# Optimization experiments

Hardware: AMD Instinct MI355X
Metric: run time of the kernel (lower is better)

The kernel has to match this reference:

```python
import jax, jax.numpy as jnp
import numpy as np

N_HEAD = 16
ROPE_BASE = 10000.0


def _rope_cache(T, head_dim):
    # half-split RoPE: cos/sin of shape [T, head_dim//2]
    half = head_dim // 2
    inv_freq = ROPE_BASE ** (-jnp.arange(half, dtype=jnp.float32) / half)
    angles = jnp.arange(T, dtype=jnp.float32)[:, None] * inv_freq[None, :]  # [T, half]
    return jnp.cos(angles), jnp.sin(angles)


def _apply_rope(x, cos, sin):
    # x: [B, H, T, D]; cos/sin: [T, D//2]
    half = x.shape[-1] // 2
    x1, x2 = x[..., :half], x[..., half:]
    c = cos[None, None, :, :]
    s = sin[None, None, :, :]
    return jnp.concatenate([x1 * c - x2 * s, x1 * s + x2 * c], axis=-1)


def setup_inputs() -> dict:
    key = jax.random.key(0)
    k1, k2, k3 = jax.random.split(key, 3)
    B, T, C = 2, 2048, 1024
    x = jax.random.normal(k1, (B, T, C), dtype=jnp.float32)
    w_attn = jax.random.normal(k2, (C, 3 * C), dtype=jnp.float32) * (C ** -0.5)
    b_attn = jnp.zeros((3 * C,), dtype=jnp.float32)
    w_proj = jax.random.normal(k3, (C, C), dtype=jnp.float32) * (C ** -0.5)
    b_proj = jnp.zeros((C,), dtype=jnp.float32)
    return {"x": x, "w_attn": w_attn, "b_attn": b_attn, "w_proj": w_proj, "b_proj": b_proj}


def reference(x, w_attn, b_attn, w_proj, b_proj):
    B, T, C = x.shape
    H = N_HEAD
    hd = C // H

    qkv = x @ w_attn + b_attn                      # [B, T, 3C] fused QKV
    q, k, v = jnp.split(qkv, 3, axis=-1)
    q = q.reshape(B, T, H, hd).transpose(0, 2, 1, 3)  # [B, H, T, hd]
    k = k.reshape(B, T, H, hd).transpose(0, 2, 1, 3)
    v = v.reshape(B, T, H, hd).transpose(0, 2, 1, 3)

    cos, sin = _rope_cache(T, hd)
    q = _apply_rope(q, cos, sin)
    k = _apply_rope(k, cos, sin)

    scale = 1.0 / jnp.sqrt(jnp.float32(hd))
    att = jnp.einsum("bhqd,bhkd->bhqk", q, k) * scale  # [B, H, T, T]
    causal = jnp.tril(jnp.ones((T, T), dtype=bool))
    att = jnp.where(causal[None, None], att, -jnp.inf)
    att = jax.nn.softmax(att, axis=-1)
    y = jnp.einsum("bhqk,bhkd->bhqd", att, v)          # [B, H, T, hd]
    y = y.transpose(0, 2, 1, 3).reshape(B, T, C)
    return y @ w_proj + b_proj
```

## Files before the change

kernel.cpp:

```cpp
#include <hip/hip_runtime.h>
#include <hip/hip_bf16.h>
#include <cmath>

typedef _Float16 half_t;
typedef half_t half4 __attribute__((ext_vector_type(4)));
typedef half_t half8 __attribute__((ext_vector_type(8)));
typedef float f32x4 __attribute__((ext_vector_type(4)));

#define N_HEADS 16
#define HD      64
#define T_SEQ   2048
#define B_SZ    2
#define C_DIM   1024
#define M_ROWS  (B_SZ * T_SEQ)
#define N_QKV   (3 * C_DIM)
#define QSCALE  0.18033688f

__device__ inline void load_lds16(const half_t* g, half_t* l) {
  __builtin_amdgcn_global_load_lds(
      (const __attribute__((address_space(1))) void*)g,
      (__attribute__((address_space(3))) void*)l, 16, 0, 0);
}

__global__ __launch_bounds__(256) void k_prep(const float* __restrict__ x,
                                              half_t* __restrict__ xb,
                                              const float* __restrict__ wa,
                                              half_t* __restrict__ wT,
                                              const float* __restrict__ wp,
                                              half_t* __restrict__ wpT) {
  __shared__ float tile[64][65];
  int bid = blockIdx.x, tid = threadIdx.x;
  if (bid < 4096) {
    int i = (bid * 256 + tid) * 4;
    float4 v = *(const float4*)(x + i);
    half_t o[4] = {(half_t)v.x, (half_t)v.y, (half_t)v.z, (half_t)v.w};
    *(ulong1*)(xb + i) = *(ulong1*)o;
    return;
  }
  const float* in; half_t* out; int K, N, id;
  if (bid < 4096 + 768) { id = bid - 4096; in = wa; out = wT;  K = 1024; N = 3072; }
  else                  { id = bid - 4864; in = wp; out = wpT; K = 1024; N = 1024; }
  int n0 = (id % (N / 64)) * 64, k0 = (id / (N / 64)) * 64;
  int tx = tid & 63, ty = tid >> 6;
  #pragma unroll
  for (int i = 0; i < 64; i += 4)
    tile[ty + i][tx] = in[(size_t)(k0 + ty + i) * N + n0 + tx];
  __syncthreads();
  #pragma unroll
  for (int i = 0; i < 64; i += 4) {
    int r = ty + i;
    out[(size_t)(n0 + r) * K + k0 + tx] = (half_t)tile[tx][r];
  }
}

template <typename OT, int TN>
__global__ __launch_bounds__(256) void k_gemm(const half_t* __restrict__ A,
                                              const half_t* __restrict__ Bt,
                                              const float* __restrict__ bias,
                                              OT* __restrict__ C,
                                              int M, int N, int K) {
  constexpr int NI = TN / 32;
  __shared__ half_t As[128 * 64];
  __shared__ half_t Bs[TN * 64];
  int tid = threadIdx.x;
  int wave = tid >> 6, lane = tid & 63;
  int lane15 = lane & 15, quad = lane >> 4;
  int wm = (wave >> 1) * 64, wn = (wave & 1) * (TN / 2);
  int bm0 = blockIdx.y * 128, bn0 = blockIdx.x * TN;
  f32x4 acc[4][NI] = {};

  for (int kb = 0; kb < K; kb += 64) {
    const half_t* Ag = A + (size_t)bm0 * K + kb;
    const half_t* Bg = Bt + (size_t)bn0 * K + kb;
    __syncthreads();
    #pragma unroll
    for (int p = 0; p < 4; p++) {
      int fc = wave * 4 * 64 + p * 64 + lane;
      int r = fc >> 3, c = (fc & 7) ^ (r & 7);
      load_lds16(Ag + (size_t)r * K + c * 8, As + (wave * 4 + p) * 512);
    }
    #pragma unroll
    for (int p = 0; p < NI; p++) {
      int fc = wave * NI * 64 + p * 64 + lane;
      int r = fc >> 3, c = (fc & 7) ^ (r & 7);
      load_lds16(Bg + (size_t)r * K + c * 8, Bs + (wave * NI + p) * 512);
    }
    __syncthreads();
    #pragma unroll
    for (int ks = 0; ks < 2; ks++) {
      half8 af[4], bf[NI];
      #pragma unroll
      for (int i = 0; i < 4; i++) {
        int Ra = wm + i * 16 + lane15;
        af[i] = *(const half8*)(As + Ra * 64 + ((ks * 4 + quad) ^ (Ra & 7)) * 8);
      }
      #pragma unroll
      for (int i = 0; i < NI; i++) {
        int Rb = wn + i * 16 + lane15;
        bf[i] = *(const half8*)(Bs + Rb * 64 + ((ks * 4 + quad) ^ (Rb & 7)) * 8);
      }
      #pragma unroll
      for (int mi = 0; mi < 4; mi++)
        #pragma unroll
        for (int ni = 0; ni < NI; ni++)
          acc[mi][ni] = __builtin_amdgcn_mfma_f32_16x16x32_f16(af[mi], bf[ni], acc[mi][ni], 0, 0, 0);
    }
  }
  #pragma unroll
  for (int mi = 0; mi < 4; mi++)
    #pragma unroll
    for (int ni = 0; ni < NI; ni++) {
      int n = bn0 + wn + ni * 16 + lane15;
      float bv = bias[n];
      int mrow = bm0 + wm + mi * 16 + quad * 4;
      #pragma unroll
      for (int r = 0; r < 4; r++)
        C[(size_t)(mrow + r) * N + n] = (OT)(acc[mi][ni][r] + bv);
    }
}

__global__ __launch_bounds__(256) void k_rope(const half_t* __restrict__ qkv,
                                              half_t* __restrict__ Q,
                                              half_t* __restrict__ Ko,
                                              half_t* __restrict__ Vt) {
  __shared__ float vt[64][65];
  int bh = blockIdx.y;
  int b = bh >> 4, h = bh & 15;
  int t0 = blockIdx.x * 64;
  int tid = threadIdx.x;
  int trow = tid >> 5, i = tid & 31;
  float inv = exp2f(-(float)i * (13.287712379549449f / 32.0f));
  #pragma unroll
  for (int p = 0; p < 8; p++) {
    int tloc = p * 8 + trow;
    int t = t0 + tloc;
    const half_t* row = qkv + (size_t)(b * T_SEQ + t) * N_QKV;
    float q1 = (float)row[h * 64 + i],        q2 = (float)row[h * 64 + i + 32];
    float k1 = (float)row[1024 + h * 64 + i], k2 = (float)row[1024 + h * 64 + i + 32];
    float v1 = (float)row[2048 + h * 64 + i], v2 = (float)row[2048 + h * 64 + i + 32];
    float s, c;
    sincosf((float)t * inv, &s, &c);
    size_t base = ((size_t)bh * T_SEQ + t) * HD;
    Q[base + i]       = (half_t)((q1 * c - q2 * s) * QSCALE);
    Q[base + i + 32]  = (half_t)((q1 * s + q2 * c) * QSCALE);
    Ko[base + i]      = (half_t)(k1 * c - k2 * s);
    Ko[base + i + 32] = (half_t)(k1 * s + k2 * c);
    vt[i][tloc]      = v1;
    vt[i + 32][tloc] = v2;
  }
  __syncthreads();
  int d = tid >> 6, tc = tid & 63;
  #pragma unroll
  for (int p = 0; p < 16; p++) {
    int dd = p * 4 + d;
    Vt[((size_t)bh * HD + dd) * T_SEQ + t0 + tc] = (half_t)vt[dd][tc];
  }
}

template <bool DIAG>
__device__ __forceinline__ void tile_mfma(const half_t* __restrict__ Kt,
                                          const half_t* __restrict__ Vt,
                                          half8 bq0, half8 bq1,
                                          f32x4 (&ot)[4], float& l,
                                          int lane15, int quad, int qloc) {
  f32x4 sacc[4];
  #pragma unroll
  for (int s = 0; s < 4; s++) {
    int R_ = s * 16 + lane15;
    half8 ak0 = *(const half8*)(Kt + R_ * 64 + ((quad) ^ (R_ & 7)) * 8);
    half8 ak1 = *(const half8*)(Kt + R_ * 64 + ((4 + quad) ^ (R_ & 7)) * 8);
    f32x4 z = {};
    z = __builtin_amdgcn_mfma_f32_16x16x32_f16(ak0, bq0, z, 0, 0, 0);
    sacc[s] = __builtin_amdgcn_mfma_f32_16x16x32_f16(ak1, bq1, z, 0, 0, 0);
  }
  #pragma unroll
  for (int s = 0; s < 4; s++) {
    half4 bp;
    #pragma unroll
    for (int r = 0; r < 4; r++) {
      float sv = sacc[s][r];
      if (DIAG && (s * 16 + quad * 4 + r > qloc)) sv = -1.0e30f;
      float p = exp2f(fminf(sv, 14.0f));
      l += p;
      bp[r] = (half_t)p;
    }
    #pragma unroll
    for (int nm = 0; nm < 4; nm++) {
      int Rv = nm * 16 + lane15;
      half4 av = *(const half4*)(Vt + Rv * 64 +
                                 ((2 * s + (quad >> 1)) ^ (Rv & 7)) * 8 +
                                 (quad & 1) * 4);
      ot[nm] = __builtin_amdgcn_mfma_f32_16x16x16f16(av, bp, ot[nm], 0, 0, 0);
    }
  }
}

#define STAGE(bb, t_)                                                          \
  {                                                                            \
    int gS = wave >> 3;                                                        \
    int idx = (wave & 7) * 64 + lane;                                          \
    int rr_ = idx >> 3, cc = (idx & 7) ^ (rr_ & 7);                            \
    int j = 2 * (t_) + gS;                                                     \
    load_lds16(Kb + (size_t)(j * 64 + rr_) * HD + cc * 8,                      \
               &KV[bb][0][gS][0] + idx * 8);                                   \
    load_lds16(Vb + (size_t)rr_ * T_SEQ + j * 64 + cc * 8,                     \
               &KV[bb][1][gS][0] + idx * 8);                                   \
  }

__device__ __forceinline__ void process_tile(
    int qt, const half_t* __restrict__ Qb, const half_t* __restrict__ Kb,
    const half_t* __restrict__ Vb, half_t* __restrict__ y, int b, int h,
    half_t (&KV)[2][2][2][4096],
    int wave, int lane, int g, int wq, int lane15, int quad) {
  int q0 = qt * 128;
  int qrow = q0 + wq * 16 + lane15;
  half8 bq0 = *(const half8*)(Qb + (size_t)qrow * HD + quad * 8);
  half8 bq1 = *(const half8*)(Qb + (size_t)qrow * HD + 32 + quad * 8);
  f32x4 ot[4] = {};
  float l = 0.f;
  int R = qt + 1;
  for (int r = 0; r < R - 1; r++) {
    __syncthreads();
    STAGE((r + 1) & 1, r + 1);
    tile_mfma<false>(&KV[r & 1][0][g][0], &KV[r & 1][1][g][0], bq0, bq1, ot, l,
                     lane15, quad, 0);
  }
  __syncthreads();
  {
    int buf = (R - 1) & 1;
    const half_t* Kt = &KV[buf][0][g][0];
    const half_t* Vt = &KV[buf][1][g][0];
    if (g == 0)
      tile_mfma<true>(Kt, Vt, bq0, bq1, ot, l, lane15, quad, wq * 16 + lane15);
    else if (wq >= 4)
      tile_mfma<true>(Kt, Vt, bq0, bq1, ot, l, lane15, quad,
                      (wq - 4) * 16 + lane15);
  }
  l += __shfl_xor(l, 16);
  l += __shfl_xor(l, 32);
  __syncthreads();
  float* cb = (float*)&KV[0][0][0][0];
  int ci = (wq * 64 + lane) * 17;
  if (g == 1) {
    #pragma unroll
    for (int nm = 0; nm < 4; nm++)
      #pragma unroll
      for (int r = 0; r < 4; r++) cb[ci + nm * 4 + r] = ot[nm][r];
    cb[ci + 16] = l;
  }
  __syncthreads();
  if (g == 0) {
    #pragma unroll
    for (int nm = 0; nm < 4; nm++)
      #pragma unroll
      for (int r = 0; r < 4; r++) ot[nm][r] += cb[ci + nm * 4 + r];
    l += cb[ci + 16];
    float invl = 1.0f / l;
    int t = q0 + wq * 16 + lane15;
    half_t* yr = y + (size_t)(b * T_SEQ + t) * C_DIM + h * 64;
    #pragma unroll
    for (int nm = 0; nm < 4; nm++) {
      half4 o4;
      #pragma unroll
      for (int r = 0; r < 4; r++) o4[r] = (half_t)(ot[nm][r] * invl);
      *(half4*)(yr + nm * 16 + quad * 4) = o4;
    }
  }
  __syncthreads();
}

__global__ __launch_bounds__(1024, 4) void k_flash(const half_t* __restrict__ Qg,
                                                   const half_t* __restrict__ Kg,
                                                   const half_t* __restrict__ Vg,
                                                   half_t* __restrict__ y) {
  __shared__ half_t KV[2][2][2][4096];
  int bh = blockIdx.y;
  int b = bh >> 4, h = bh & 15;
  int x = blockIdx.x;
  int tid = threadIdx.x;
  int wave = tid >> 6, lane = tid & 63;
  int g = wave >> 3, wq = wave & 7;
  int lane15 = lane & 15, quad = lane >> 4;
  const half_t* Qb = Qg + (size_t)bh * T_SEQ * HD;
  const half_t* Kb = Kg + (size_t)bh * T_SEQ * HD;
  const half_t* Vb = Vg + (size_t)bh * HD * T_SEQ;

  int qtA = x, qtB = 15 - x;
  STAGE(0, 0);
  process_tile(qtA, Qb, Kb, Vb, y, b, h, KV, wave, lane, g, wq, lane15, quad);
  STAGE(0, 0);
  process_tile(qtB, Qb, Kb, Vb, y, b, h, KV, wave, lane, g, wq, lane15, quad);
  #undef STAGE
}

extern "C" void kernel_launch(void* const* d_in, const int* in_sizes, int n_in,
                              void* d_out, int out_size, void* d_ws, size_t ws_size,
                              hipStream_t stream) {
  const float* x      = (const float*)d_in[0];
  const float* w_attn = (const float*)d_in[1];
  const float* b_attn = (const float*)d_in[2];
  const float* w_proj = (const float*)d_in[3];
  const float* b_proj = (const float*)d_in[4];
  float* out = (float*)d_out;

  char* ws = (char*)d_ws;
  const size_t MB = 1u << 20;
  half_t* xb  = (half_t*)(ws);
  half_t* wT  = (half_t*)(ws + 8 * MB);
  half_t* wpT = (half_t*)(ws + 14 * MB);
  half_t* Q   = (half_t*)(ws + 16 * MB);
  half_t* Kb  = (half_t*)(ws + 24 * MB);
  half_t* Vt  = (half_t*)(ws + 32 * MB);
  half_t* qkv = (half_t*)(ws + 40 * MB);
  half_t* y   = (half_t*)(ws + 40 * MB);

  k_prep<<<4096 + 768 + 256, 256, 0, stream>>>(x, xb, w_attn, wT, w_proj, wpT);
  k_gemm<half_t, 128><<<dim3(N_QKV / 128, M_ROWS / 128), 256, 0, stream>>>(
      xb, wT, b_attn, qkv, M_ROWS, N_QKV, C_DIM);
  k_rope<<<dim3(T_SEQ / 64, B_SZ * N_HEADS), 256, 0, stream>>>(qkv, Q, Kb, Vt);
  k_flash<<<dim3(8, B_SZ * N_HEADS), 1024, 0, stream>>>(Q, Kb, Vt, y);
  k_gemm<float, 64><<<dim3(C_DIM / 64, M_ROWS / 128), 256, 0, stream>>>(
      y, wpT, b_proj, out, M_ROWS, C_DIM, C_DIM);
}
```

Before: 185.1 us.

## Fuse RoPE and V tiling into QKV GEMM epilogue with precomputed sincos table

The separate RoPE kernel is removed. Its work moves into a dedicated QKV GEMM epilogue, which applies the rotation using a cos/sin table built in the prep kernel and writes Q, K and a tiled V layout directly. This drops the fp16 qkv round trip through global memory and one kernel launch. The V layout changes to 64x64 tiles per key block, so the flash kernel's V staging address is updated to match. The cost is a more complex epilogue with scattered writes and table loads, plus an extra LDS transpose pass for the V blocks.

```diff
diff --git a/kernel.cpp b/kernel.cpp
--- a/kernel.cpp
+++ b/kernel.cpp
@@ -27,7 +27,8 @@
                                               const float* __restrict__ wa,
                                               half_t* __restrict__ wT,
                                               const float* __restrict__ wp,
-                                              half_t* __restrict__ wpT) {
+                                              half_t* __restrict__ wpT,
+                                              float2* __restrict__ tbl) {
   __shared__ float tile[64][65];
   int bid = blockIdx.x, tid = threadIdx.x;
   if (bid < 4096) {
@@ -37,9 +38,18 @@
     *(ulong1*)(xb + i) = *(ulong1*)o;
     return;
   }
+  if (bid >= 5120) {
+    int idx = (bid - 5120) * 256 + tid;
+    int t = idx >> 5, j = idx & 31;
+    float inv = exp2f(-(float)j * (13.287712379549449f / 32.0f));
+    float s, c;
+    sincosf((float)t * inv, &s, &c);
+    tbl[idx] = make_float2(c, s);
+    return;
+  }
   const float* in; half_t* out; int K, N, id;
-  if (bid < 4096 + 768) { id = bid - 4096; in = wa; out = wT;  K = 1024; N = 3072; }
-  else                  { id = bid - 4864; in = wp; out = wpT; K = 1024; N = 1024; }
+  if (bid < 4864) { id = bid - 4096; in = wa; out = wT;  K = 1024; N = 3072; }
+  else            { id = bid - 4864; in = wp; out = wpT; K = 1024; N = 1024; }
   int n0 = (id % (N / 64)) * 64, k0 = (id / (N / 64)) * 64;
   int tx = tid & 63, ty = tid >> 6;
   #pragma unroll
@@ -119,41 +129,118 @@
     }
 }
 
-__global__ __launch_bounds__(256) void k_rope(const half_t* __restrict__ qkv,
-                                              half_t* __restrict__ Q,
-                                              half_t* __restrict__ Ko,
-                                              half_t* __restrict__ Vt) {
-  __shared__ float vt[64][65];
-  int bh = blockIdx.y;
-  int b = bh >> 4, h = bh & 15;
-  int t0 = blockIdx.x * 64;
+__global__ __launch_bounds__(256) void k_gemm_qkv(const half_t* __restrict__ A,
+                                                  const half_t* __restrict__ Bt,
+                                                  const float* __restrict__ bias,
+                                                  const float2* __restrict__ tbl,
+                                                  half_t* __restrict__ Qo,
+                                                  half_t* __restrict__ Ko,
+                                                  half_t* __restrict__ Vo) {
+  __shared__ half_t smem[16640];
+  half_t* As = smem;
+  half_t* Bs = smem + 8192;
   int tid = threadIdx.x;
-  int trow = tid >> 5, i = tid & 31;
-  float inv = exp2f(-(float)i * (13.287712379549449f / 32.0f));
-  #pragma unroll
-  for (int p = 0; p < 8; p++) {
-    int tloc = p * 8 + trow;
-    int t = t0 + tloc;
-    const half_t* row = qkv + (size_t)(b * T_SEQ + t) * N_QKV;
-    float q1 = (float)row[h * 64 + i],        q2 = (float)row[h * 64 + i + 32];
-    float k1 = (float)row[1024 + h * 64 + i], k2 = (float)row[1024 + h * 64 + i + 32];
-    float v1 = (float)row[2048 + h * 64 + i], v2 = (float)row[2048 + h * 64 + i + 32];
-    float s, c;
-    sincosf((float)t * inv, &s, &c);
-    size_t base = ((size_t)bh * T_SEQ + t) * HD;
-    Q[base + i]       = (half_t)((q1 * c - q2 * s) * QSCALE);
-    Q[base + i + 32]  = (half_t)((q1 * s + q2 * c) * QSCALE);
-    Ko[base + i]      = (half_t)(k1 * c - k2 * s);
-    Ko[base + i + 32] = (half_t)(k1 * s + k2 * c);
-    vt[i][tloc]      = v1;
-    vt[i + 32][tloc] = v2;
-  }
-  __syncthreads();
-  int d = tid >> 6, tc = tid & 63;
-  #pragma unroll
-  for (int p = 0; p < 16; p++) {
-    int dd = p * 4 + d;
-    Vt[((size_t)bh * HD + dd) * T_SEQ + t0 + tc] = (half_t)vt[dd][tc];
+  int wave = tid >> 6, lane = tid & 63;
+  int lane15 = lane & 15, quad = lane >> 4;
+  int wm = (wave >> 1) * 64, wn = (wave & 1) * 64;
+  int bm0 = blockIdx.y * 128, bn0 = blockIdx.x * 128;
+  f32x4 acc[4][4] = {};
+
+  for (int kb = 0; kb < C_DIM; kb += 64) {
+    const half_t* Ag = A + (size_t)bm0 * C_DIM + kb;
+    const half_t* Bg = Bt + (size_t)bn0 * C_DIM + kb;
+    __syncthreads();
+    #pragma unroll
+    for (int p = 0; p < 4; p++) {
+      int fc = wave * 4 * 64 + p * 64 + lane;
+      int r = fc >> 3, c = (fc & 7) ^ (r & 7);
+      load_lds16(Ag + (size_t)r * C_DIM + c * 8, As + (wave * 4 + p) * 512);
+    }
+    #pragma unroll
+    for (int p = 0; p < 4; p++) {
+      int fc = wave * 4 * 64 + p * 64 + lane;
+      int r = fc >> 3, c = (fc & 7) ^ (r & 7);
+      load_lds16(Bg + (size_t)r * C_DIM + c * 8, Bs + (wave * 4 + p) * 512);
+    }
+    __syncthreads();
+    #pragma unroll
+    for (int ks = 0; ks < 2; ks++) {
+      half8 af[4], bf[4];
+      #pragma unroll
+      for (int i = 0; i < 4; i++) {
+        int Ra = wm + i * 16 + lane15;
+        af[i] = *(const half8*)(As + Ra * 64 + ((ks * 4 + quad) ^ (Ra & 7)) * 8);
+      }
+      #pragma unroll
+      for (int i = 0; i < 4; i++) {
+        int Rb = wn + i * 16 + lane15;
+        bf[i] = *(const half8*)(Bs + Rb * 64 + ((ks * 4 + quad) ^ (Rb & 7)) * 8);
+      }
+      #pragma unroll
+      for (int mi = 0; mi < 4; mi++)
+        #pragma unroll
+        for (int ni = 0; ni < 4; ni++)
+          acc[mi][ni] = __builtin_amdgcn_mfma_f32_16x16x32_f16(af[mi], bf[ni], acc[mi][ni], 0, 0, 0);
+    }
+  }
+  #pragma unroll
+  for (int ni = 0; ni < 4; ni++) {
+    float bv = bias[bn0 + wn + ni * 16 + lane15];
+    #pragma unroll
+    for (int mi = 0; mi < 4; mi++)
+      #pragma unroll
+      for (int r = 0; r < 4; r++) acc[mi][ni][r] += bv;
+  }
+
+  int third = bn0 >> 10;
+  if (third < 2) {
+    half_t* Ob = (third == 0) ? Qo : Ko;
+    int h = ((bn0 & 1023) + wn) >> 6;
+    #pragma unroll
+    for (int mi = 0; mi < 4; mi++) {
+      int mrow = bm0 + wm + mi * 16 + quad * 4;
+      int bq = mrow >> 11, tq = mrow & 2047;
+      half_t* outp = Ob + ((size_t)(bq * 16 + h) * T_SEQ + tq) * HD;
+      #pragma unroll
+      for (int p = 0; p < 2; p++) {
+        int j = p * 16 + lane15;
+        #pragma unroll
+        for (int r = 0; r < 4; r++) {
+          float2 cs = tbl[(tq + r) * 32 + j];
+          float a1 = acc[mi][p][r], a2 = acc[mi][p + 2][r];
+          float o1 = a1 * cs.x - a2 * cs.y;
+          float o2 = a1 * cs.y + a2 * cs.x;
+          if (third == 0) { o1 *= QSCALE; o2 *= QSCALE; }
+          outp[r * HD + j]      = (half_t)o1;
+          outp[r * HD + j + 32] = (half_t)o2;
+        }
+      }
+    }
+  } else {
+    __syncthreads();
+    #pragma unroll
+    for (int mi = 0; mi < 4; mi++)
+      #pragma unroll
+      for (int ni = 0; ni < 4; ni++) {
+        int tl = wm + mi * 16 + quad * 4, nl = wn + ni * 16 + lane15;
+        #pragma unroll
+        for (int r = 0; r < 4; r++)
+          smem[(tl + r) * 130 + nl] = (half_t)acc[mi][ni][r];
+      }
+    __syncthreads();
+    int hV = (bn0 - 2048) >> 6;
+    int bq = bm0 >> 11, tq0 = bm0 & 2047;
+    int c8 = (tid & 7) * 8;
+    #pragma unroll
+    for (int p = 0; p < 8; p++) {
+      int gr = p * 32 + (tid >> 3);
+      int tb = gr & 1, d = (gr >> 1) & 63, h2 = gr >> 7;
+      half8 vv;
+      #pragma unroll
+      for (int jj = 0; jj < 8; jj++)
+        vv[jj] = smem[(tb * 64 + c8 + jj) * 130 + h2 * 64 + d];
+      *(half8*)(Vo + ((size_t)((bq * 16 + hV + h2) * 32 + (tq0 >> 6) + tb) * 64 + d) * 64 + c8) = vv;
+    }
   }
 }
 
@@ -203,7 +290,7 @@
     int j = 2 * (t_) + gS;                                                     \
     load_lds16(Kb + (size_t)(j * 64 + rr_) * HD + cc * 8,                      \
                &KV[bb][0][gS][0] + idx * 8);                                   \
-    load_lds16(Vb + (size_t)rr_ * T_SEQ + j * 64 + cc * 8,                     \
+    load_lds16(Vb + (size_t)j * 4096 + rr_ * 64 + cc * 8,                      \
                &KV[bb][1][gS][0] + idx * 8);                                   \
   }
 
@@ -311,13 +398,13 @@
   half_t* Q   = (half_t*)(ws + 16 * MB);
   half_t* Kb  = (half_t*)(ws + 24 * MB);
   half_t* Vt  = (half_t*)(ws + 32 * MB);
-  half_t* qkv = (half_t*)(ws + 40 * MB);
   half_t* y   = (half_t*)(ws + 40 * MB);
-
-  k_prep<<<4096 + 768 + 256, 256, 0, stream>>>(x, xb, w_attn, wT, w_proj, wpT);
-  k_gemm<half_t, 128><<<dim3(N_QKV / 128, M_ROWS / 128), 256, 0, stream>>>(
-      xb, wT, b_attn, qkv, M_ROWS, N_QKV, C_DIM);
-  k_rope<<<dim3(T_SEQ / 64, B_SZ * N_HEADS), 256, 0, stream>>>(qkv, Q, Kb, Vt);
+  float2* tbl = (float2*)(ws + 48 * MB);
+
+  k_prep<<<4096 + 768 + 256 + 256, 256, 0, stream>>>(x, xb, w_attn, wT,
+                                                     w_proj, wpT, tbl);
+  k_gemm_qkv<<<dim3(N_QKV / 128, M_ROWS / 128), 256, 0, stream>>>(
+      xb, wT, b_attn, tbl, Q, Kb, Vt);
   k_flash<<<dim3(8, B_SZ * N_HEADS), 1024, 0, stream>>>(Q, Kb, Vt, y);
   k_gemm<float, 64><<<dim3(C_DIM / 64, M_ROWS / 128), 256, 0, stream>>>(
       y, wpT, b_proj, out, M_ROWS, C_DIM, C_DIM);
```

Result: no change. 185.6 us (+0.3%).
